# Kernel optimization log

Hardware: AMD Instinct MI355X
Metric: run time of the kernel (lower is better)

The kernel has to match this reference:

```python
import math
import jax, jax.numpy as jnp
import numpy as np

B, T, D = 4, 2048, 768
NH, DH = 12, 64

def setup_inputs() -> dict:
    key = jax.random.key(0)
    k1, k2, k3 = jax.random.split(key, 3)
    scale_attn = 1.0 / math.sqrt(D)
    scale_proj = 1.0 / math.sqrt(D)
    return {
        "x": jax.random.normal(k1, (B, T, D), dtype=jnp.float32),
        "w_attn": jax.random.normal(k2, (D, 3 * D), dtype=jnp.float32) * scale_attn,
        "b_attn": jnp.zeros((3 * D,), dtype=jnp.float32),
        "w_proj": jax.random.normal(k3, (D, D), dtype=jnp.float32) * scale_proj,
        "b_proj": jnp.zeros((D,), dtype=jnp.float32),
    }

def reference(x, w_attn, b_attn, w_proj, b_proj):
    Bx, Tx, Dx = x.shape
    qkv = x @ w_attn + b_attn                     # [B, T, 3D]
    q, k, v = jnp.split(qkv, 3, axis=-1)          # each [B, T, D]
    # [B, T, D] -> [B, NH, T, DH]
    def to_heads(t):
        return t.reshape(Bx, Tx, NH, DH).transpose(0, 2, 1, 3)
    q, k, v = to_heads(q), to_heads(k), to_heads(v)
    attn = jnp.einsum("bhqd,bhkd->bhqk", q, k) / math.sqrt(DH)
    causal = jnp.tril(jnp.ones((Tx, Tx), dtype=bool))
    attn = jnp.where(causal[None, None, :, :], attn, -jnp.inf)
    attn = jax.nn.softmax(attn, axis=-1)
    out = jnp.einsum("bhqk,bhkd->bhqd", attn, v)  # [B, NH, T, DH]
    out = out.transpose(0, 2, 1, 3).reshape(Bx, Tx, Dx)
    out = out @ w_proj + b_proj
    return (out, (k, v))
```

## Files before the change

kernel.cpp:

```cpp
#include <hip/hip_runtime.h>
#include <hip/hip_bf16.h>

typedef unsigned short ushort_t;
typedef __attribute__((ext_vector_type(8))) short short8;
typedef __attribute__((ext_vector_type(4))) float f32x4;

#define B_    4
#define T_    2048
#define D_    768
#define NH_   12
#define DH_   64
#define KDIM  768

__device__ __forceinline__ ushort_t f2bf(float f) {
  union { float f; unsigned u; } c; c.f = f;
  unsigned u = c.u;
  return (ushort_t)((u + 0x7FFFu + ((u >> 16) & 1u)) >> 16);
}

__device__ __forceinline__ unsigned cvt_pk_bf16(float lo, float hi) {
  unsigned r;
  asm("v_cvt_pk_bf16_f32 %0, %1, %2" : "=v"(r) : "v"(lo), "v"(hi));
  return r;
}

__device__ __forceinline__ void gload_lds16(const void* g, void* l) {
  __builtin_amdgcn_global_load_lds(
      (const __attribute__((address_space(1))) unsigned int*)g,
      (__attribute__((address_space(3))) unsigned int*)l, 16, 0, 0);
}

__global__ void cvt_bf16_vec(const float* __restrict__ in,
                             ushort_t* __restrict__ out, int n4) {
  int i = blockIdx.x * blockDim.x + threadIdx.x;
  if (i >= n4) return;
  float4 v = ((const float4*)in)[i];
  ushort4 o;
  o.x = f2bf(v.x); o.y = f2bf(v.y); o.z = f2bf(v.z); o.w = f2bf(v.w);
  ((ushort4*)out)[i] = o;
}

__global__ void transpose_cvt(const float* __restrict__ in,
                              ushort_t* __restrict__ out, int R, int C) {
  __shared__ float tile[32][33];
  int c0 = blockIdx.x * 32, r0 = blockIdx.y * 32;
  int tx = threadIdx.x, ty = threadIdx.y;
#pragma unroll
  for (int j = 0; j < 32; j += 8)
    tile[ty + j][tx] = in[(size_t)(r0 + ty + j) * C + c0 + tx];
  __syncthreads();
#pragma unroll
  for (int j = 0; j < 32; j += 8)
    out[(size_t)(c0 + ty + j) * R + r0 + tx] = f2bf(tile[tx][ty + j]);
}

__device__ __forceinline__ void gemm128_mainloop(
    const ushort_t* __restrict__ A, const ushort_t* __restrict__ BT,
    int m0, int n0, ushort_t* lds, f32x4 acc[4][4]) {
  const int t = threadIdx.x;
  const int l = t & 63;
  const int w = t >> 6;
  const int wm = w >> 1, wn = w & 1;
  const int g = l >> 4, qi = l & 15;
  const int c0 = t, c1 = t + 256;
  const int r0 = c0 >> 2, r1 = c1 >> 2;
  const int s0 = (c0 & 3) ^ ((r0 >> 2) & 3);
  const int s1 = (c1 & 3) ^ ((r1 >> 2) & 3);
  const ushort_t* ga0 = A + (size_t)(m0 + r0) * KDIM + (s0 << 3);
  const ushort_t* ga1 = A + (size_t)(m0 + r1) * KDIM + (s1 << 3);
  const ushort_t* gb0 = BT + (size_t)(n0 + r0) * KDIM + (s0 << 3);
  const ushort_t* gb1 = BT + (size_t)(n0 + r1) * KDIM + (s1 << 3);
  const int NK = KDIM / 32;
  const int rsw = (g ^ qi >> 2) << 3;

  gload_lds16(ga0, lds + w * 512);
  gload_lds16(ga1, lds + 2048 + w * 512);
  gload_lds16(gb0, lds + 4096 + w * 512);
  gload_lds16(gb1, lds + 6144 + w * 512);

  for (int kk = 0; kk < NK; ++kk) {
    asm volatile("s_waitcnt vmcnt(0)" ::: "memory");
    __builtin_amdgcn_sched_barrier(0);
    __builtin_amdgcn_s_barrier();
    __builtin_amdgcn_sched_barrier(0);
    if (kk + 1 < NK) {
      ushort_t* ln = lds + ((kk + 1) & 1) * 8192;
      int k0 = (kk + 1) * 32;
      gload_lds16(ga0 + k0, ln + w * 512);
      gload_lds16(ga1 + k0, ln + 2048 + w * 512);
      gload_lds16(gb0 + k0, ln + 4096 + w * 512);
      gload_lds16(gb1 + k0, ln + 6144 + w * 512);
    }
    ushort_t* lb = lds + (kk & 1) * 8192;
    short8 af[4], bfv[4];
#pragma unroll
    for (int mt = 0; mt < 4; ++mt)
      af[mt] = *(const short8*)&lb[(wm * 64 + mt * 16 + qi) * 32 + rsw];
#pragma unroll
    for (int nt = 0; nt < 4; ++nt)
      bfv[nt] = *(const short8*)&lb[4096 + (wn * 64 + nt * 16 + qi) * 32 + rsw];
#pragma unroll
    for (int mt = 0; mt < 4; ++mt)
#pragma unroll
      for (int nt = 0; nt < 4; ++nt)
        acc[mt][nt] = __builtin_amdgcn_mfma_f32_16x16x32_bf16(
            af[mt], bfv[nt], acc[mt][nt], 0, 0, 0);
  }
}

__global__ __launch_bounds__(256) void gemm_qkv_kernel(
    const ushort_t* __restrict__ xbf, const ushort_t* __restrict__ wT,
    const float* __restrict__ bias, ushort_t* __restrict__ qbf,
    float* __restrict__ kout, float* __restrict__ vout,
    ushort_t* __restrict__ kbf, ushort_t* __restrict__ vtbf) {
  __shared__ ushort_t lds[16384];
  int bid = blockIdx.x;
  int m0 = (bid & 63) << 7;
  int n0 = (bid >> 6) << 7;
  f32x4 acc[4][4];
  f32x4 zero = {0.f, 0.f, 0.f, 0.f};
#pragma unroll
  for (int a = 0; a < 4; ++a)
#pragma unroll
    for (int b = 0; b < 4; ++b) acc[a][b] = zero;
  gemm128_mainloop(xbf, wT, m0, n0, lds, acc);

  const float QSC = 0.125f * 1.44269504089f;
  const int l = threadIdx.x & 63, w = threadIdx.x >> 6;
  const int wm = w >> 1, wn = w & 1;
  const int sec = n0 / 768;
  const int b = m0 >> 11;
  const int tt_base = (m0 & 2047) + wm * 64;
#pragma unroll
  for (int nt = 0; nt < 4; ++nt) {
    int n = n0 + wn * 64 + nt * 16 + (l & 15);
    float bv = bias[n];
    int nn = n - sec * 768;
    int h = nn >> 6, dh = nn & 63;
    size_t head_base = ((size_t)(b * NH_ + h) * T_);
#pragma unroll
    for (int mt = 0; mt < 4; ++mt) {
      int tt0 = tt_base + mt * 16 + ((l >> 4) << 2);
      float vals[4];
#pragma unroll
      for (int r = 0; r < 4; ++r) vals[r] = acc[mt][nt][r] + bv;
      if (sec == 0) {
#pragma unroll
        for (int r = 0; r < 4; ++r)
          qbf[((head_base + tt0 + r) << 6) + dh] = f2bf(vals[r] * QSC);
      } else if (sec == 1) {
#pragma unroll
        for (int r = 0; r < 4; ++r) {
          size_t idx = ((head_base + tt0 + r) << 6) + dh;
          kout[idx] = vals[r];
          kbf[idx] = f2bf(vals[r]);
        }
      } else {
#pragma unroll
        for (int r = 0; r < 4; ++r)
          vout[((head_base + tt0 + r) << 6) + dh] = vals[r];
        ushort4 pk;
        pk.x = f2bf(vals[0]); pk.y = f2bf(vals[1]);
        pk.z = f2bf(vals[2]); pk.w = f2bf(vals[3]);
        *(ushort4*)&vtbf[((size_t)(b * NH_ + h) * DH_ + dh) * T_ + tt0] = pk;
      }
    }
  }
}

__global__ __launch_bounds__(256) void gemm_proj_kernel(
    const ushort_t* __restrict__ abf, const ushort_t* __restrict__ wT,
    const float* __restrict__ bias, float* __restrict__ out) {
  __shared__ ushort_t lds[16384];
  int bid = blockIdx.x;
  int m0 = (bid & 63) << 7;
  int n0 = (bid >> 6) << 7;
  f32x4 acc[4][4];
  f32x4 zero = {0.f, 0.f, 0.f, 0.f};
#pragma unroll
  for (int a = 0; a < 4; ++a)
#pragma unroll
    for (int b = 0; b < 4; ++b) acc[a][b] = zero;
  gemm128_mainloop(abf, wT, m0, n0, lds, acc);

  const int l = threadIdx.x & 63, w = threadIdx.x >> 6;
  const int wm = w >> 1, wn = w & 1;
#pragma unroll
  for (int nt = 0; nt < 4; ++nt) {
    int n = n0 + wn * 64 + nt * 16 + (l & 15);
    float bv = bias[n];
#pragma unroll
    for (int mt = 0; mt < 4; ++mt) {
#pragma unroll
      for (int r = 0; r < 4; ++r) {
        int m = m0 + wm * 64 + mt * 16 + ((l >> 4) << 2) + r;
        out[(size_t)m * D_ + n] = acc[mt][nt][r] + bv;
      }
    }
  }
}

__device__ __forceinline__ void strip_exp_store(
    f32x4 s4[4], int gq, bool diag, int kvb, int g, int qi, char* pbase) {
  if (diag) {
#pragma unroll
    for (int nt = 0; nt < 4; ++nt)
#pragma unroll
      for (int r = 0; r < 4; ++r) {
        int gk = kvb + nt * 16 + g * 4 + r;
        if (gk > gq) s4[nt][r] = -1e30f;
      }
  }
#pragma unroll
  for (int nt = 0; nt < 4; ++nt) {
    float p0 = exp2f(s4[nt][0]);
    float p1 = exp2f(s4[nt][1]);
    float p2 = exp2f(s4[nt][2]);
    float p3 = exp2f(s4[nt][3]);
    uint2 pk;
    pk.x = cvt_pk_bf16(p0, p1);
    pk.y = cvt_pk_bf16(p2, p3);
    *(uint2*)(pbase + ((nt * 32 + g * 8) ^ ((qi & 7) << 4))) = pk;
  }
}

__global__ __launch_bounds__(512, 6) void attn_fwd_kernel(
    const ushort_t* __restrict__ qbf, const ushort_t* __restrict__ kbf,
    const ushort_t* __restrict__ vtbf, ushort_t* __restrict__ obf) {
  __shared__ ushort_t Kl[2][4096];
  __shared__ ushort_t Vt[2][4096];
  __shared__ ushort_t Pl[8][1024];
  const int bid = blockIdx.x;
  const int swz = (bid & 7) * 96 + (bid >> 3);
  const int jp = swz & 15;
  const int bh = swz >> 4;
  const int qlo = jp << 6, qhi = (31 - jp) << 6;
  const int lastH = 31 - jp, lastL = jp;
  const int t = threadIdx.x, l = t & 63, w = t >> 6;
  const int g = l >> 4, qi = l & 15;
  const bool isHi = (w < 4);
  const int wc = isHi ? w : (w - 4);
  const int qs0 = (isHi ? qhi : qlo) + wc * 16;
  const int lastMe = isHi ? lastH : lastL;

  const ushort_t* Qb = qbf + (size_t)bh * T_ * DH_;
  const ushort_t* Kb = kbf + (size_t)bh * T_ * DH_;
  const ushort_t* Vb = vtbf + (size_t)bh * DH_ * T_;

  const int row0 = t >> 3, ch0 = t & 7;
  const ushort_t* gK0 = Kb + row0 * DH_ + ((ch0 ^ (row0 & 7)) << 3);
  const ushort_t* gV0 = Vb + (size_t)row0 * T_ + ((ch0 ^ (row0 & 7)) << 3);

  short8 aq[2];
  {
    const int qr = qs0 + qi;
    aq[0] = *(const short8*)&Qb[(size_t)qr * DH_ + (g << 3)];
    aq[1] = *(const short8*)&Qb[(size_t)qr * DH_ + (g << 3) + 32];
  }

  short8 ones;
#pragma unroll
  for (int j = 0; j < 8; ++j) ones[j] = (short)0x3F80;

  f32x4 o[4], al;
  f32x4 zero = {0.f, 0.f, 0.f, 0.f};
#pragma unroll
  for (int nt = 0; nt < 4; ++nt) o[nt] = zero;
  al = zero;

  gload_lds16(gK0, &Kl[0][w * 512]);
  gload_lds16(gV0, &Vt[0][w * 512]);

  char* pb = (char*)&Pl[w][0] + qi * 128;

  for (int kt = 0; kt <= lastH; ++kt) {
    const int buf = kt & 1;
    const int kvb = kt << 6;
    asm volatile("s_waitcnt vmcnt(0)" ::: "memory");
    __builtin_amdgcn_sched_barrier(0);
    __builtin_amdgcn_s_barrier();
    __builtin_amdgcn_sched_barrier(0);
    if (kt < lastH) {
      const int nx = kt + 1;
      gload_lds16(gK0 + (size_t)nx * 4096, &Kl[buf ^ 1][w * 512]);
      gload_lds16(gV0 + (size_t)nx * 64, &Vt[buf ^ 1][w * 512]);
    }
    if (kt <= lastMe) {
      f32x4 s4[4];
#pragma unroll
      for (int nt = 0; nt < 4; ++nt) s4[nt] = zero;
#pragma unroll
      for (int h2 = 0; h2 < 2; ++h2) {
#pragma unroll
        for (int nt = 0; nt < 4; ++nt) {
          short8 bk = *(const short8*)&Kl[buf][((nt * 16 + qi) << 6) +
                                              (((g + 4 * h2) ^ (qi & 7)) << 3)];
          s4[nt] = __builtin_amdgcn_mfma_f32_16x16x32_bf16(bk, aq[h2],
                                                           s4[nt], 0, 0, 0);
        }
      }
      strip_exp_store(s4, qs0 + qi, kt == lastMe, kvb, g, qi, pb);
#pragma unroll
      for (int k2 = 0; k2 < 2; ++k2) {
        short8 pf = *(const short8*)(pb + ((g * 16 + k2 * 64) ^ ((qi & 7) << 4)));
#pragma unroll
        for (int nt = 0; nt < 4; ++nt) {
          short8 av = *(const short8*)&Vt[buf][((nt * 16 + qi) << 6) +
                                               (((g + 4 * k2) ^ (qi & 7)) << 3)];
          o[nt] = __builtin_amdgcn_mfma_f32_16x16x32_bf16(av, pf, o[nt],
                                                          0, 0, 0);
        }
        al = __builtin_amdgcn_mfma_f32_16x16x32_bf16(ones, pf, al, 0, 0, 0);
      }
    }
  }

  const int b = bh / NH_, h = bh - b * NH_;
  {
    float inv = 1.f / al[0];
    int q = qs0 + qi;
    size_t rowb = (size_t)(b * T_ + q) * D_ + h * DH_;
#pragma unroll
    for (int nt = 0; nt < 4; ++nt) {
      ushort4 pk;
      pk.x = f2bf(o[nt][0] * inv);
      pk.y = f2bf(o[nt][1] * inv);
      pk.z = f2bf(o[nt][2] * inv);
      pk.w = f2bf(o[nt][3] * inv);
      *(ushort4*)&obf[rowb + nt * 16 + g * 4] = pk;
    }
  }
}

extern "C" void kernel_launch(void* const* d_in, const int* in_sizes, int n_in,
                              void* d_out, int out_size, void* d_ws, size_t ws_size,
                              hipStream_t stream) {
  const float* x      = (const float*)d_in[0];
  const float* w_attn = (const float*)d_in[1];
  const float* b_attn = (const float*)d_in[2];
  const float* w_proj = (const float*)d_in[3];
  const float* b_proj = (const float*)d_in[4];

  float* out  = (float*)d_out;
  float* kout = out + (size_t)B_ * T_ * D_;
  float* vout = kout + (size_t)B_ * T_ * D_;

  char* ws = (char*)d_ws;
  ushort_t* xbf = (ushort_t*)(ws);
  ushort_t* wTa = (ushort_t*)(ws + 12582912);
  ushort_t* wTp = (ushort_t*)(ws + 16121856);
  ushort_t* qbf = (ushort_t*)(ws + 17301504);
  ushort_t* kbf = (ushort_t*)(ws + 29884416);
  ushort_t* vtbf = (ushort_t*)(ws + 42467328);
  ushort_t* abf = xbf;

  cvt_bf16_vec<<<6144, 256, 0, stream>>>(x, xbf, (B_ * T_ * D_) / 4);
  dim3 tb(32, 8);
  transpose_cvt<<<dim3(72, 24), tb, 0, stream>>>(w_attn, wTa, D_, 3 * D_);
  transpose_cvt<<<dim3(24, 24), tb, 0, stream>>>(w_proj, wTp, D_, D_);

  gemm_qkv_kernel<<<64 * 18, 256, 0, stream>>>(xbf, wTa, b_attn, qbf, kout, vout,
                                               kbf, vtbf);
  attn_fwd_kernel<<<768, 512, 0, stream>>>(qbf, kbf, vtbf, abf);
  gemm_proj_kernel<<<64 * 6, 256, 0, stream>>>(abf, wTp, b_proj, out);
}
```

Before: 140.6 us.

## Triple-buffer GEMM mainloop LDS and reorder tile mapping for weight reuse

The shared GEMM mainloop moves from double-buffered to triple-buffered LDS staging. Loads for tile k+2 are issued while tile k is computed, and the wait becomes vmcnt(4) so one tile of loads can stay in flight. Both GEMM kernels also change the block index mapping so consecutive blocks walk along N for the same M rows, which should improve L2 reuse of the activation rows. LDS per block grows from 32KB to 48KB, which may reduce occupancy.

```diff
diff --git a/kernel.cpp b/kernel.cpp
--- a/kernel.cpp
+++ b/kernel.cpp
@@ -73,25 +73,36 @@
   const int NK = KDIM / 32;
   const int rsw = (g ^ qi >> 2) << 3;
 
-  gload_lds16(ga0, lds + w * 512);
-  gload_lds16(ga1, lds + 2048 + w * 512);
-  gload_lds16(gb0, lds + 4096 + w * 512);
-  gload_lds16(gb1, lds + 6144 + w * 512);
-
+#pragma unroll
+  for (int p = 0; p < 2; ++p) {
+    ushort_t* lp = lds + p * 8192;
+    int k0 = p * 32;
+    gload_lds16(ga0 + k0, lp + w * 512);
+    gload_lds16(ga1 + k0, lp + 2048 + w * 512);
+    gload_lds16(gb0 + k0, lp + 4096 + w * 512);
+    gload_lds16(gb1 + k0, lp + 6144 + w * 512);
+  }
+
+  int kb = 0;
   for (int kk = 0; kk < NK; ++kk) {
-    asm volatile("s_waitcnt vmcnt(0)" ::: "memory");
+    if (kk < NK - 1) {
+      asm volatile("s_waitcnt vmcnt(4)" ::: "memory");
+    } else {
+      asm volatile("s_waitcnt vmcnt(0)" ::: "memory");
+    }
     __builtin_amdgcn_sched_barrier(0);
     __builtin_amdgcn_s_barrier();
     __builtin_amdgcn_sched_barrier(0);
-    if (kk + 1 < NK) {
-      ushort_t* ln = lds + ((kk + 1) & 1) * 8192;
-      int k0 = (kk + 1) * 32;
-      gload_lds16(ga0 + k0, ln + w * 512);
-      gload_lds16(ga1 + k0, ln + 2048 + w * 512);
-      gload_lds16(gb0 + k0, ln + 4096 + w * 512);
-      gload_lds16(gb1 + k0, ln + 6144 + w * 512);
-    }
-    ushort_t* lb = lds + (kk & 1) * 8192;
+    if (kk + 2 < NK) {
+      int kb2 = kb + 2 >= 3 ? kb - 1 : kb + 2;
+      ushort_t* lp = lds + kb2 * 8192;
+      int k0 = (kk + 2) * 32;
+      gload_lds16(ga0 + k0, lp + w * 512);
+      gload_lds16(ga1 + k0, lp + 2048 + w * 512);
+      gload_lds16(gb0 + k0, lp + 4096 + w * 512);
+      gload_lds16(gb1 + k0, lp + 6144 + w * 512);
+    }
+    ushort_t* lb = lds + kb * 8192;
     short8 af[4], bfv[4];
 #pragma unroll
     for (int mt = 0; mt < 4; ++mt)
@@ -105,6 +116,7 @@
       for (int nt = 0; nt < 4; ++nt)
         acc[mt][nt] = __builtin_amdgcn_mfma_f32_16x16x32_bf16(
             af[mt], bfv[nt], acc[mt][nt], 0, 0, 0);
+    kb = kb + 1 >= 3 ? 0 : kb + 1;
   }
 }
 
@@ -113,10 +125,10 @@
     const float* __restrict__ bias, ushort_t* __restrict__ qbf,
     float* __restrict__ kout, float* __restrict__ vout,
     ushort_t* __restrict__ kbf, ushort_t* __restrict__ vtbf) {
-  __shared__ ushort_t lds[16384];
+  __shared__ ushort_t lds[24576];
   int bid = blockIdx.x;
-  int m0 = (bid & 63) << 7;
-  int n0 = (bid >> 6) << 7;
+  int m0 = (bid / 18) << 7;
+  int n0 = (bid % 18) << 7;
   f32x4 acc[4][4];
   f32x4 zero = {0.f, 0.f, 0.f, 0.f};
 #pragma unroll
@@ -171,10 +183,10 @@
 __global__ __launch_bounds__(256) void gemm_proj_kernel(
     const ushort_t* __restrict__ abf, const ushort_t* __restrict__ wT,
     const float* __restrict__ bias, float* __restrict__ out) {
-  __shared__ ushort_t lds[16384];
+  __shared__ ushort_t lds[24576];
   int bid = blockIdx.x;
-  int m0 = (bid & 63) << 7;
-  int n0 = (bid >> 6) << 7;
+  int m0 = (bid / 6) << 7;
+  int n0 = (bid % 6) << 7;
   f32x4 acc[4][4];
   f32x4 zero = {0.f, 0.f, 0.f, 0.f};
 #pragma unroll
```

After: 141.8 us. Within noise of the previous version (+0.8%).
